# Optimization experiments

Hardware: AMD Instinct MI355X
Metric: run time of the kernel (lower is better)

The kernel has to match this reference:

```python
import jax, jax.numpy as jnp
import numpy as np

N_SPK, N_UTT, D_EMB = 1024, 20, 512
COS_EPS = 1e-8   # torch F.cosine_similarity default eps
SIM_EPS = 1e-6   # added to cosine and inside the log, per original code


def setup_inputs() -> dict:
    key = jax.random.key(0)
    embeddings = jax.random.normal(key, (N_SPK, N_UTT, D_EMB), dtype=jnp.float32)
    w = jnp.asarray(10.0, dtype=jnp.float32)
    b = jnp.asarray(-5.0, dtype=jnp.float32)
    return {"embeddings": embeddings, "w": w, "b": b}


def reference(embeddings, w, b):
    N, M, D = embeddings.shape
    sums = embeddings.sum(axis=1)                       # [N, D]
    centroids = sums / M                                # [N, D] full centroids
    cent_excl = (sums[:, None, :] - embeddings) / (M - 1)  # [N, M, D] leave-one-out

    def _norm(x):
        return x / jnp.maximum(jnp.linalg.norm(x, axis=-1, keepdims=True), COS_EPS)

    e_n = _norm(embeddings)          # [N, M, D]
    c_n = _norm(centroids)           # [N, D]
    ce_n = _norm(cent_excl)          # [N, M, D]

    # cosine vs every speaker centroid
    cs = jnp.einsum('nmd,kd->nmk', e_n, c_n)            # [N, M, N]
    # replace same-speaker column with leave-one-out cosine
    diag = jnp.sum(e_n * ce_n, axis=-1)                 # [N, M]
    same = jnp.eye(N, dtype=bool)[:, None, :]           # [N, 1, N]
    cossim = jnp.where(same, diag[:, :, None], cs) + SIM_EPS

    sim = w * cossim + b                                # [N, M, N]
    pos = w * (diag + SIM_EPS) + b                      # sim[j, i, j]
    lse = jnp.log(jnp.sum(jnp.exp(sim), axis=-1) + SIM_EPS)  # [N, M]
    loss = jnp.sum(lse - pos)
    return loss
```

## Files before the change

### kernel.cpp

```cpp
#include <hip/hip_runtime.h>
#include <hip/hip_bf16.h>

typedef unsigned short u16;
typedef unsigned int u32;
typedef unsigned char u8;
typedef int i32x8 __attribute__((ext_vector_type(8)));
typedef float f32x4 __attribute__((ext_vector_type(4)));

#define NSPK 1024
#define NUTT 20
#define DEMB 512
#define NROW (NSPK * NUTT)

__device__ __forceinline__ uint2 pk_fp8x8(float a, float b, float c, float d,
                                          float e, float f, float g, float h) {
    int lo = __builtin_amdgcn_cvt_pk_fp8_f32(a, b, 0, 0);
    lo = __builtin_amdgcn_cvt_pk_fp8_f32(c, d, lo, 1);
    int hi = __builtin_amdgcn_cvt_pk_fp8_f32(e, f, 0, 0);
    hi = __builtin_amdgcn_cvt_pk_fp8_f32(g, h, hi, 1);
    return make_uint2((u32)lo, (u32)hi);
}

__global__ __launch_bounds__(256) void prep_f(const float* __restrict__ E,
                                              u8* __restrict__ A,
                                              u8* __restrict__ Bc,
                                              float* __restrict__ diag,
                                              float* __restrict__ csd,
                                              float* __restrict__ rs,
                                              float* __restrict__ out) {
    __shared__ float sbuf[4][DEMB];
    const int t = threadIdx.x, lane = t & 63, wv = t >> 6;
    const int n = blockIdx.x;
    const float* Eb = E + (size_t)n * (NUTT * DEMB) + (size_t)(wv * 5) * DEMB + lane * 8;

    float4 e0[5], e1[5];
    float4 p0 = {0, 0, 0, 0}, p1 = {0, 0, 0, 0};
#pragma unroll
    for (int i = 0; i < 5; ++i) {
        e0[i] = *(const float4*)(Eb + (size_t)i * DEMB);
        e1[i] = *(const float4*)(Eb + (size_t)i * DEMB + 4);
        p0.x += e0[i].x; p0.y += e0[i].y; p0.z += e0[i].z; p0.w += e0[i].w;
        p1.x += e1[i].x; p1.y += e1[i].y; p1.z += e1[i].z; p1.w += e1[i].w;
    }
    *(float4*)(&sbuf[wv][lane * 8])     = p0;
    *(float4*)(&sbuf[wv][lane * 8 + 4]) = p1;
    __syncthreads();

    float4 s0 = {0, 0, 0, 0}, s1 = {0, 0, 0, 0};
#pragma unroll
    for (int k = 0; k < 4; ++k) {
        float4 a = *(const float4*)(&sbuf[k][lane * 8]);
        float4 b = *(const float4*)(&sbuf[k][lane * 8 + 4]);
        s0.x += a.x; s0.y += a.y; s0.z += a.z; s0.w += a.w;
        s1.x += b.x; s1.y += b.y; s1.z += b.z; s1.w += b.w;
    }

    float ls = s0.x*s0.x + s0.y*s0.y + s0.z*s0.z + s0.w*s0.w
             + s1.x*s1.x + s1.y*s1.y + s1.z*s1.z + s1.w*s1.w;
#pragma unroll
    for (int o = 32; o; o >>= 1) ls += __shfl_xor(ls, o);
    const float ss = ls;
    const float rc = 1.0f / fmaxf(sqrtf(ss) * 0.05f, 1e-8f);
    const float g  = rc * 0.05f;

    ((uint2*)(Bc + (size_t)n * DEMB))[lane] =
        pk_fp8x8(s0.x * g, s0.y * g, s0.z * g, s0.w * g,
                 s1.x * g, s1.y * g, s1.z * g, s1.w * g);

#pragma unroll
    for (int i = 0; i < 5; ++i) {
        float ee = e0[i].x*e0[i].x + e0[i].y*e0[i].y + e0[i].z*e0[i].z + e0[i].w*e0[i].w
                 + e1[i].x*e1[i].x + e1[i].y*e1[i].y + e1[i].z*e1[i].z + e1[i].w*e1[i].w;
        float es = e0[i].x*s0.x + e0[i].y*s0.y + e0[i].z*s0.z + e0[i].w*s0.w
                 + e1[i].x*s1.x + e1[i].y*s1.y + e1[i].z*s1.z + e1[i].w*s1.w;
#pragma unroll
        for (int o = 32; o; o >>= 1) { ee += __shfl_xor(ee, o); es += __shfl_xor(es, o); }

        const float rne = 1.0f / fmaxf(sqrtf(ee), 1e-8f);
        const float pxx = ss - 2.f * es + ee;
        const float dg  = (es - ee) * rne / fmaxf(sqrtf(pxx), 1.9e-7f);

        const int r = n * NUTT + wv * 5 + i;
        ((uint2*)(A + (size_t)r * DEMB))[lane] =
            pk_fp8x8(e0[i].x * rne, e0[i].y * rne, e0[i].z * rne, e0[i].w * rne,
                     e1[i].x * rne, e1[i].y * rne, e1[i].z * rne, e1[i].w * rne);
        if (lane == 0) {
            diag[r] = dg;
            csd[r]  = es * g * rne;
        }
    }

    if (t < NUTT) rs[n * NUTT + t] = 0.f;
    if (n == 0 && t == 0) out[0] = 0.f;
}

__device__ __forceinline__ void async_copy16(const void* g, void* l) {
    __builtin_amdgcn_global_load_lds(
        (const __attribute__((address_space(1))) void*)g,
        (__attribute__((address_space(3))) void*)l, 16, 0, 0);
}

__global__ __launch_bounds__(256) void gemm_mx(const u8* __restrict__ A,
                                               const u8* __restrict__ Bc,
                                               const float* __restrict__ wp,
                                               const float* __restrict__ bp,
                                               float* __restrict__ rowsum) {
    __shared__ u8 As[128 * 128];
    __shared__ u8 Bs[128 * 128];
    const int t = threadIdx.x;
    const int lane = t & 63, wv = t >> 6;
    const int ml = lane & 15, q = lane >> 4;
    const int wm = wv >> 1, wn = wv & 1;
    const int tileM = blockIdx.x;
    const int tileN = blockIdx.y;

    const float w = *wp, bb = *bp;

    const u8* Ag = A + (size_t)tileM * 128 * DEMB;
    const u8* Bg = Bc + (size_t)tileN * 128 * DEMB;

    const u8* asrc[4]; const u8* bsrc[4]; u8* adst[4]; u8* bdst[4];
#pragma unroll
    for (int j = 0; j < 4; ++j) {
        const int c = t + 256 * j;
        const int r = c >> 3, kg = (c & 7) ^ (r & 7);
        asrc[j] = Ag + (size_t)r * DEMB + kg * 16;  adst[j] = As + c * 16;
        bsrc[j] = Bg + (size_t)r * DEMB + kg * 16;  bdst[j] = Bs + c * 16;
    }

    int a0[4], a1[4], b0[4], b1[4];
#pragma unroll
    for (int i = 0; i < 4; ++i) {
        const int r = wm * 64 + i * 16 + ml;
        const int c = wn * 64 + i * 16 + ml;
        a0[i] = r * 128 + (((2 * q)     ^ (r & 7)) << 4);
        a1[i] = r * 128 + (((2 * q + 1) ^ (r & 7)) << 4);
        b0[i] = c * 128 + (((2 * q)     ^ (c & 7)) << 4);
        b1[i] = c * 128 + (((2 * q + 1) ^ (c & 7)) << 4);
    }

    f32x4 acc[4][4];
#pragma unroll
    for (int i = 0; i < 4; ++i)
#pragma unroll
        for (int j = 0; j < 4; ++j) acc[i][j] = (f32x4){0.f, 0.f, 0.f, 0.f};

    for (int kt = 0; kt < DEMB; kt += 128) {
        __syncthreads();
#pragma unroll
        for (int j = 0; j < 4; ++j) async_copy16(asrc[j] + kt, adst[j]);
#pragma unroll
        for (int j = 0; j < 4; ++j) async_copy16(bsrc[j] + kt, bdst[j]);
        __syncthreads();

        i32x8 af[4], bf[4];
#pragma unroll
        for (int i = 0; i < 4; ++i) {
            uint4 x = *(const uint4*)(As + a0[i]);
            uint4 y = *(const uint4*)(As + a1[i]);
            af[i] = (i32x8){(int)x.x, (int)x.y, (int)x.z, (int)x.w,
                            (int)y.x, (int)y.y, (int)y.z, (int)y.w};
        }
#pragma unroll
        for (int j = 0; j < 4; ++j) {
            uint4 x = *(const uint4*)(Bs + b0[j]);
            uint4 y = *(const uint4*)(Bs + b1[j]);
            bf[j] = (i32x8){(int)x.x, (int)x.y, (int)x.z, (int)x.w,
                            (int)y.x, (int)y.y, (int)y.z, (int)y.w};
        }
#pragma unroll
        for (int i = 0; i < 4; ++i)
#pragma unroll
            for (int j = 0; j < 4; ++j)
                acc[i][j] = __builtin_amdgcn_mfma_scale_f32_16x16x128_f8f6f4(
                    af[i], bf[j], acc[i][j], 0, 0,
                    0, 0x7F7F7F7F, 0, 0x7F7F7F7F);
    }

#pragma unroll
    for (int i = 0; i < 4; ++i) {
        float s0 = 0.f, s1 = 0.f, s2 = 0.f, s3 = 0.f;
#pragma unroll
        for (int j = 0; j < 4; ++j) {
            s0 += __expf(fmaf(w, acc[i][j][0] + 1e-6f, bb));
            s1 += __expf(fmaf(w, acc[i][j][1] + 1e-6f, bb));
            s2 += __expf(fmaf(w, acc[i][j][2] + 1e-6f, bb));
            s3 += __expf(fmaf(w, acc[i][j][3] + 1e-6f, bb));
        }
#pragma unroll
        for (int o = 1; o < 16; o <<= 1) {
            s0 += __shfl_xor(s0, o); s1 += __shfl_xor(s1, o);
            s2 += __shfl_xor(s2, o); s3 += __shfl_xor(s3, o);
        }
        if (ml < 4) {
            float sv = (ml == 0) ? s0 : (ml == 1) ? s1 : (ml == 2) ? s2 : s3;
            int grow = tileM * 128 + wm * 64 + i * 16 + q * 4 + ml;
            atomicAdd(&rowsum[grow], sv);
        }
    }
}

__global__ __launch_bounds__(256) void finalize(const float* __restrict__ rowsum,
                                                const float* __restrict__ diag,
                                                const float* __restrict__ csd,
                                                const float* __restrict__ wp,
                                                const float* __restrict__ bp,
                                                float* __restrict__ out) {
    __shared__ float s_red[4];
    const int r = blockIdx.x * 256 + threadIdx.x;
    const float w = *wp, bb = *bp;
    const float dg = diag[r];
    const float pos = fmaf(w, dg + 1e-6f, bb);
    const float S = rowsum[r] - __expf(fmaf(w, csd[r] + 1e-6f, bb)) + __expf(pos);
    float term = logf(S + 1e-6f) - pos;
    const int lane = threadIdx.x & 63, wv = threadIdx.x >> 6;
#pragma unroll
    for (int o = 32; o; o >>= 1) term += __shfl_xor(term, o);
    if (lane == 0) s_red[wv] = term;
    __syncthreads();
    if (threadIdx.x == 0) atomicAdd(out, s_red[0] + s_red[1] + s_red[2] + s_red[3]);
}

extern "C" void kernel_launch(void* const* d_in, const int* in_sizes, int n_in,
                              void* d_out, int out_size, void* d_ws, size_t ws_size,
                              hipStream_t stream) {
    const float* E = (const float*)d_in[0];
    const float* wp = (const float*)d_in[1];
    const float* bp = (const float*)d_in[2];
    float* out = (float*)d_out;

    char* ws = (char*)d_ws;
    u8* A      = (u8*)(ws);
    u8* Bc     = (u8*)(ws + 10485760);
    float* dg  = (float*)(ws + 11010048);
    float* cs  = (float*)(ws + 11091968);
    float* rs  = (float*)(ws + 11173888);

    prep_f<<<NSPK, 256, 0, stream>>>(E, A, Bc, dg, cs, rs, out);
    gemm_mx<<<dim3(160, 8), 256, 0, stream>>>(A, Bc, wp, bp, rs);
    finalize<<<80, 256, 0, stream>>>(rs, dg, cs, wp, bp, out);
}
```

Before: 109.6 us.

## Widen GEMM tile to 128x256 and fuse finalize via last-block counter

The GEMM block grows to 512 threads and covers 256 centroid columns instead of 128. This halves the grid along N and halves how often each A tile is reloaded. The separate finalize kernel is removed: each row tile keeps an atomic counter, and the last of the four column blocks to finish computes the log-sum-exp terms and adds them to the output. This saves one kernel launch but adds a threadfence, a counter atomic and more LDS per block, which may lower occupancy.

```diff
diff --git a/kernel.cpp b/kernel.cpp
--- a/kernel.cpp
+++ b/kernel.cpp
@@ -27,6 +27,7 @@
                                               float* __restrict__ diag,
                                               float* __restrict__ csd,
                                               float* __restrict__ rs,
+                                              int* __restrict__ cnt,
                                               float* __restrict__ out) {
     __shared__ float sbuf[4][DEMB];
     const int t = threadIdx.x, lane = t & 63, wv = t >> 6;
@@ -91,6 +92,7 @@
     }
 
     if (t < NUTT) rs[n * NUTT + t] = 0.f;
+    if (n == 0 && t < 160) cnt[t] = 0;
     if (n == 0 && t == 0) out[0] = 0.f;
 }
 
@@ -100,31 +102,43 @@
         (__attribute__((address_space(3))) void*)l, 16, 0, 0);
 }
 
-__global__ __launch_bounds__(256) void gemm_mx(const u8* __restrict__ A,
+__global__ __launch_bounds__(512) void gemm_mx(const u8* __restrict__ A,
                                                const u8* __restrict__ Bc,
                                                const float* __restrict__ wp,
                                                const float* __restrict__ bp,
-                                               float* __restrict__ rowsum) {
+                                               float* __restrict__ rowsum,
+                                               const float* __restrict__ diag,
+                                               const float* __restrict__ csd,
+                                               int* __restrict__ cnt,
+                                               float* __restrict__ out) {
     __shared__ u8 As[128 * 128];
-    __shared__ u8 Bs[128 * 128];
+    __shared__ u8 Bs[256 * 128];
+    __shared__ float s_red[8];
+    __shared__ int s_old;
     const int t = threadIdx.x;
     const int lane = t & 63, wv = t >> 6;
     const int ml = lane & 15, q = lane >> 4;
-    const int wm = wv >> 1, wn = wv & 1;
+    const int wm = wv >> 2, wn = wv & 3;
     const int tileM = blockIdx.x;
     const int tileN = blockIdx.y;
 
     const float w = *wp, bb = *bp;
 
     const u8* Ag = A + (size_t)tileM * 128 * DEMB;
-    const u8* Bg = Bc + (size_t)tileN * 128 * DEMB;
-
-    const u8* asrc[4]; const u8* bsrc[4]; u8* adst[4]; u8* bdst[4];
-#pragma unroll
-    for (int j = 0; j < 4; ++j) {
-        const int c = t + 256 * j;
+    const u8* Bg = Bc + (size_t)tileN * 256 * DEMB;
+
+    const u8* asrc[2]; u8* adst[2];
+#pragma unroll
+    for (int j = 0; j < 2; ++j) {
+        const int c = t + 512 * j;
         const int r = c >> 3, kg = (c & 7) ^ (r & 7);
         asrc[j] = Ag + (size_t)r * DEMB + kg * 16;  adst[j] = As + c * 16;
+    }
+    const u8* bsrc[4]; u8* bdst[4];
+#pragma unroll
+    for (int j = 0; j < 4; ++j) {
+        const int c = t + 512 * j;
+        const int r = c >> 3, kg = (c & 7) ^ (r & 7);
         bsrc[j] = Bg + (size_t)r * DEMB + kg * 16;  bdst[j] = Bs + c * 16;
     }
 
@@ -148,7 +162,7 @@
     for (int kt = 0; kt < DEMB; kt += 128) {
         __syncthreads();
 #pragma unroll
-        for (int j = 0; j < 4; ++j) async_copy16(asrc[j] + kt, adst[j]);
+        for (int j = 0; j < 2; ++j) async_copy16(asrc[j] + kt, adst[j]);
 #pragma unroll
         for (int j = 0; j < 4; ++j) async_copy16(bsrc[j] + kt, bdst[j]);
         __syncthreads();
@@ -198,27 +212,32 @@
             atomicAdd(&rowsum[grow], sv);
         }
     }
-}
-
-__global__ __launch_bounds__(256) void finalize(const float* __restrict__ rowsum,
-                                                const float* __restrict__ diag,
-                                                const float* __restrict__ csd,
-                                                const float* __restrict__ wp,
-                                                const float* __restrict__ bp,
-                                                float* __restrict__ out) {
-    __shared__ float s_red[4];
-    const int r = blockIdx.x * 256 + threadIdx.x;
-    const float w = *wp, bb = *bp;
-    const float dg = diag[r];
-    const float pos = fmaf(w, dg + 1e-6f, bb);
-    const float S = rowsum[r] - __expf(fmaf(w, csd[r] + 1e-6f, bb)) + __expf(pos);
-    float term = logf(S + 1e-6f) - pos;
-    const int lane = threadIdx.x & 63, wv = threadIdx.x >> 6;
-#pragma unroll
-    for (int o = 32; o; o >>= 1) term += __shfl_xor(term, o);
-    if (lane == 0) s_red[wv] = term;
+
+    __threadfence();
     __syncthreads();
-    if (threadIdx.x == 0) atomicAdd(out, s_red[0] + s_red[1] + s_red[2] + s_red[3]);
+    if (t == 0) s_old = atomicAdd(&cnt[tileM], 1);
+    __syncthreads();
+    if (s_old == 3) {
+        float term = 0.f;
+        if (t < 128) {
+            const int r = tileM * 128 + t;
+            const float rsv = atomicAdd(&rowsum[r], 0.0f);
+            const float dgv = diag[r];
+            const float pos = fmaf(w, dgv + 1e-6f, bb);
+            const float S = rsv - __expf(fmaf(w, csd[r] + 1e-6f, bb)) + __expf(pos);
+            term = logf(S + 1e-6f) - pos;
+        }
+#pragma unroll
+        for (int o = 32; o; o >>= 1) term += __shfl_xor(term, o);
+        if (lane == 0) s_red[wv] = term;
+        __syncthreads();
+        if (t == 0) {
+            float tot = 0.f;
+#pragma unroll
+            for (int k = 0; k < 8; ++k) tot += s_red[k];
+            atomicAdd(out, tot);
+        }
+    }
 }
 
 extern "C" void kernel_launch(void* const* d_in, const int* in_sizes, int n_in,
@@ -235,8 +254,8 @@
     float* dg  = (float*)(ws + 11010048);
     float* cs  = (float*)(ws + 11091968);
     float* rs  = (float*)(ws + 11173888);
-
-    prep_f<<<NSPK, 256, 0, stream>>>(E, A, Bc, dg, cs, rs, out);
-    gemm_mx<<<dim3(160, 8), 256, 0, stream>>>(A, Bc, wp, bp, rs);
-    finalize<<<80, 256, 0, stream>>>(rs, dg, cs, wp, bp, out);
-}
+    int* cnt   = (int*)(ws + 11255808);
+
+    prep_f<<<NSPK, 256, 0, stream>>>(E, A, Bc, dg, cs, rs, cnt, out);
+    gemm_mx<<<dim3(160, 4), 512, 0, stream>>>(A, Bc, wp, bp, rs, dg, cs, cnt, out);
+}
```

After: 177.7 us. 1.62x slower.
